# Kernel tuning notes

Measured on AMD Instinct MI355X. Metric: run time of the kernel, lower is better.

Reference implementation:

```python
import jax, jax.numpy as jnp
import numpy as np

B, C, IN_LEN, OUT_LEN, E, TOP_K, N_I = 1, 8192, 512, 512, 8, 2, 16


def setup_inputs() -> dict:
    key = jax.random.key(0)
    ks = jax.random.split(key, 8)
    w = lambda k, shape, sc=0.02: jax.random.normal(k, shape, dtype=jnp.float32) * sc
    return {
        "x": jax.random.normal(ks[0], (B, C, IN_LEN), dtype=jnp.float32),
        "Ins_tk": jax.random.normal(ks[1], (B, N_I, OUT_LEN), dtype=jnp.float32),
        "gate_w": w(ks[2], (IN_LEN, E)),            # Gate: Linear(in_len, E, bias=False)
        "expert_w": w(ks[3], (E, IN_LEN, OUT_LEN)),  # per-expert Linear weight (transposed)
        "expert_b": jnp.zeros((E, OUT_LEN), dtype=jnp.float32),
        "gamma_w": w(ks[4], (E, OUT_LEN)),          # EiLM gamma_generator: Linear(h,1,bias=False)
        "beta_w": w(ks[5], (E, OUT_LEN, OUT_LEN)),  # EiLM beta_generator (transposed)
        "rmod_w": w(ks[6], (OUT_LEN, E)),           # router_modulator: Linear(out_len, E, bias=False)
    }


def reference(x, Ins_tk, gate_w, expert_w, expert_b, gamma_w, beta_w, rmod_w):
    Bx, Cx, L = x.shape
    xf = x.reshape(-1, L)                                   # [N, in_len], N = B*C
    ins = Ins_tk[0]                                         # [N_i, out_len] (B==1 asserted)

    # Router: logits + expert-wise modulation of logits
    router_gamma = jnp.mean(ins @ rmod_w, axis=0)           # [E]
    logits = xf @ gate_w + router_gamma                     # [N, E]
    probs = jax.nn.softmax(logits.astype(jnp.float32), axis=-1)
    rw, sel = jax.lax.top_k(probs, TOP_K)                   # [N, k] values/indices (no renorm)

    # Combine weights per token per expert: sum_k rw[t,k] * onehot(sel[t,k])
    combine = jnp.sum(jax.nn.one_hot(sel, E, dtype=rw.dtype) * rw[..., None], axis=1)  # [N, E]

    # EiLM per-expert affine params: scalar gamma, vector beta (mean over instruction tokens)
    gam = jnp.mean(ins @ gamma_w.T, axis=0)                 # [E]
    bet = jnp.einsum('nh,ehd->ed', ins, beta_w) / N_I       # [E, out_len]

    # Per-expert linear over all tokens, then EiLM modulation
    eo = jnp.einsum('nl,eld->end', xf, expert_w) + expert_b[:, None, :]   # [E, N, out]
    mod = gam[:, None, None] * eo + bet[:, None, :]                        # [E, N, out]

    out = jnp.einsum('ne,end->nd', combine, mod)            # [N, out]
    return out.reshape(Bx, Cx, OUT_LEN)
```

## Files before the change

kernel.cpp:

```cpp
#include <hip/hip_runtime.h>
#include <hip/hip_bf16.h>

#define N_TOK 8192
#define INL   512
#define OUTL  512
#define NE    8
#define NI    16

typedef unsigned short ushort_t;
typedef unsigned int   uint_t;
typedef short  short8  __attribute__((ext_vector_type(8)));
typedef float  floatx4 __attribute__((ext_vector_type(4)));

#define WS_S      0u
#define WS_GAM    2048u
#define WS_RGAM   2080u
#define WS_BET    2112u
#define WS_SELE   18496u
#define WS_SELW   51264u
#define WS_WT     182336u

__device__ __forceinline__ ushort_t f2bf(float f) {
    uint_t b = __float_as_uint(f);
    return (ushort_t)((b + 0x7FFFu + ((b >> 16) & 1u)) >> 16);
}
__device__ __forceinline__ uint_t pkbf(float a, float b) {
    __hip_bfloat162 h = __float22bfloat162_rn(make_float2(a, b));
    union { __hip_bfloat162 h2; uint_t u; } cv;
    cv.h2 = h;
    return cv.u;
}
__device__ __forceinline__ void dma16(const ushort_t* g, ushort_t* l) {
    __builtin_amdgcn_global_load_lds(
        (const __attribute__((address_space(1))) void*)g,
        (__attribute__((address_space(3))) void*)l,
        16, 0, 0);
}

__global__ void k_stats(const float* __restrict__ ins,
                        const float* __restrict__ gamma_w,
                        const float* __restrict__ rmod_w,
                        float* __restrict__ wsS, float* __restrict__ wsGam,
                        float* __restrict__ wsRgam) {
    __shared__ float sS[INL];
    __shared__ float pg[64], pr[64];
    int tid = threadIdx.x;
    for (int h = tid; h < INL; h += 256) {
        float a = 0.f;
        for (int n = 0; n < NI; ++n) a += ins[n * INL + h];
        sS[h] = a;
        wsS[h] = a;
    }
    __syncthreads();
    if (tid < 64) {
        int e = tid & 7, qq = tid >> 3;
        float g = 0.f, r = 0.f;
        for (int j = 0; j < 64; ++j) {
            int h = qq * 64 + j;
            float sv = sS[h];
            g += sv * gamma_w[e * INL + h];
            r += sv * rmod_w[h * NE + e];
        }
        pg[tid] = g; pr[tid] = r;
    }
    __syncthreads();
    if (tid < NE) {
        float g = 0.f, r = 0.f;
        for (int qq = 0; qq < 8; ++qq) { g += pg[qq * 8 + tid]; r += pr[qq * 8 + tid]; }
        wsGam[tid]  = g * (1.f / NI);
        wsRgam[tid] = r * (1.f / NI);
    }
}

__global__ void k_bet(const float* __restrict__ ins,
                      const float* __restrict__ gamma_w,
                      const float* __restrict__ beta_w,
                      const float* __restrict__ expert_b,
                      float* __restrict__ wsBet) {
    __shared__ float sS[INL];
    __shared__ float red[256];
    __shared__ float gamS;
    int e = blockIdx.y;
    int dBase = blockIdx.x * 32;
    int tid = threadIdx.x;
    for (int h = tid; h < INL; h += 256) {
        float a = 0.f;
        for (int n = 0; n < NI; ++n) a += ins[n * INL + h];
        sS[h] = a;
    }
    __syncthreads();
    if (tid < 64) {
        float g = 0.f;
        for (int j = 0; j < 8; ++j) g += sS[tid * 8 + j] * gamma_w[e * INL + tid * 8 + j];
        for (int off = 32; off >= 1; off >>= 1) g += __shfl_xor(g, off, 64);
        if (tid == 0) gamS = g * (1.f / NI);
    }
    int doff = tid & 31, hq = tid >> 5;
    float a = 0.f;
    for (int j = 0; j < 64; ++j) {
        int h = hq * 64 + j;
        a += sS[h] * beta_w[(e * INL + h) * OUTL + dBase + doff];
    }
    red[tid] = a;
    __syncthreads();
    if (tid < 32) {
        float t = 0.f;
        for (int k = 0; k < 8; ++k) t += red[k * 32 + tid];
        int d = dBase + tid;
        wsBet[e * OUTL + d] = t * (1.f / NI) + gamS * expert_b[e * OUTL + d];
    }
}

__global__ void k_route(const float* __restrict__ x,
                        const float* __restrict__ gate_w,
                        const float* __restrict__ wsGam,
                        const float* __restrict__ wsRgam,
                        int* __restrict__ selE, float4* __restrict__ selW) {
    __shared__ float gateT[NE * INL];
    int tid = threadIdx.x;
    for (int i = 0; i < 16; ++i) {
        int f = tid + 256 * i;
        float v = gate_w[f];
        gateT[(f & 7) * INL + (f >> 3)] = v;
    }
    __syncthreads();

    int w = tid >> 6, lane = tid & 63;
    int tbase = blockIdx.x * 16 + w * 4;

    for (int tt = 0; tt < 4; ++tt) {
        int t = tbase + tt;
        float2 xv[4];
        for (int i = 0; i < 4; ++i)
            xv[i] = *(const float2*)(x + (size_t)t * INL + 2 * lane + 128 * i);

        float acc[NE];
        for (int e = 0; e < NE; ++e) acc[e] = 0.f;
        for (int i = 0; i < 4; ++i) {
            int c = 2 * lane + 128 * i;
            for (int e = 0; e < NE; ++e)
                acc[e] += xv[i].x * gateT[e * INL + c] + xv[i].y * gateT[e * INL + c + 1];
        }
        for (int e = 0; e < NE; ++e) {
            float a = acc[e];
            for (int off = 32; off >= 1; off >>= 1) a += __shfl_xor(a, off, 64);
            acc[e] = a;
        }
        float logit[NE];
        for (int e = 0; e < NE; ++e) logit[e] = acc[e] + wsRgam[e];

        int i0 = 0; float m0 = logit[0];
        for (int e = 1; e < NE; ++e) if (logit[e] > m0) { m0 = logit[e]; i0 = e; }
        int i1 = -1; float m1 = -3.4e38f;
        for (int e = 0; e < NE; ++e) if (e != i0 && logit[e] > m1) { m1 = logit[e]; i1 = e; }

        float S = 0.f;
        for (int e = 0; e < NE; ++e) S += expf(logit[e] - m0);
        float rw0 = 1.0f / S;
        float rw1 = expf(m1 - m0) / S;

        if (lane == 0) {
            selE[t] = i0 | (i1 << 8);
            selW[t] = make_float4(rw0 * wsGam[i0], rw1 * wsGam[i1], rw0, rw1);
        }
    }
}

__global__ void k_wt(const float* __restrict__ expert_w, ushort_t* __restrict__ wt) {
    __shared__ float tile[64][65];
    int e = blockIdx.z;
    int lt = blockIdx.y * 64, dt = blockIdx.x * 64;
    int tid = threadIdx.x;
    int dIdx = tid & 63, lq = tid >> 6;
    for (int i = 0; i < 16; ++i) {
        int l = lq * 16 + i;
        tile[l][dIdx] = expert_w[(e * INL + lt + l) * OUTL + dt + dIdx];
    }
    __syncthreads();
    int lIdx = tid & 63, dq = tid >> 6;
    for (int i = 0; i < 16; ++i) {
        int d = dq * 16 + i;
        wt[(e * OUTL + dt + d) * INL + lt + lIdx] = f2bf(tile[lIdx][d]);
    }
}

__global__ __launch_bounds__(256, 2)
void k_gemm(const float* __restrict__ x, const ushort_t* __restrict__ wt,
            const int* __restrict__ selE, const float4* __restrict__ selW,
            const float* __restrict__ wsBet, float* __restrict__ out) {
    int bx = blockIdx.x;
    int rt = bx & 63;
    int ct = bx >> 6;
    __shared__ ushort_t Blds[2][64 * 64];

    int tid = threadIdx.x;
    int wid = tid >> 6, lane = tid & 63;
    int wm = wid * 32;
    int mrow = lane & 15, laneq = lane >> 4, q8 = laneq * 8, qr = laneq * 4;

    float wv[2][NE];
    for (int mt = 0; mt < 2; ++mt) {
        int tok = rt * 128 + wm + mt * 16 + mrow;
        int es = selE[tok];
        float4 w4 = selW[tok];
        int e0 = es & 255, e1 = es >> 8;
        for (int e = 0; e < NE; ++e)
            wv[mt][e] = (e == e0) ? w4.x : ((e == e1) ? w4.y : 0.f);
    }

    const float* arow[2];
    for (int mt = 0; mt < 2; ++mt)
        arow[mt] = x + (size_t)(rt * 128 + wm + mt * 16 + mrow) * INL + q8;

    int c0 = tid, c1 = tid + 256;
    int col0 = c0 >> 3, kg0 = ((c0 & 7) - col0) & 7;
    int col1 = c1 >> 3, kg1 = ((c1 & 7) - col1) & 7;
    const ushort_t* pB0 = wt + (size_t)(ct * 64 + col0) * INL + kg0 * 8;
    const ushort_t* pB1 = wt + (size_t)(ct * 64 + col1) * INL + kg1 * 8;
    ushort_t* ldsW0;
    ushort_t* ldsW1;
    {
        int base0 = (wid * 64) * 8;
        int base1 = (256 + wid * 64) * 8;
        ldsW0 = &Blds[0][0] + base0;
        ldsW1 = &Blds[0][0] + base1;
    }

    int fcol[4], frot0[4];
    for (int nt = 0; nt < 4; ++nt) {
        fcol[nt] = nt * 16 + mrow;
        frot0[nt] = (laneq + fcol[nt]) & 7;
    }

    floatx4 comb[2][4];
    for (int mt = 0; mt < 2; ++mt)
        for (int nt = 0; nt < 4; ++nt)
            comb[mt][nt] = (floatx4){0.f, 0.f, 0.f, 0.f};

    dma16(pB0, ldsW0);
    dma16(pB1, ldsW1);
    __syncthreads();

    float4 ar[2][2][2];

    #pragma unroll 1
    for (int kc = 0; kc < 8; ++kc) {
        for (int mt = 0; mt < 2; ++mt)
            for (int ks = 0; ks < 2; ++ks) {
                const float* p = arow[mt] + kc * 64 + ks * 32;
                ar[mt][ks][0] = *(const float4*)p;
                ar[mt][ks][1] = *(const float4*)(p + 4);
            }

        #pragma unroll
        for (int e = 0; e < NE; ++e) {
            int step = kc * 8 + e;
            int buf = step & 1;
            int ne = e + 1, nkc = kc;
            if (ne == NE) { ne = 0; nkc = kc + 1; }
            if (nkc < 8) {
                size_t off = (size_t)ne * (OUTL * INL) + (size_t)nkc * 64;
                int nb = (step + 1) & 1;
                dma16(pB0 + off, ldsW0 + nb * (64 * 64));
                dma16(pB1 + off, ldsW1 + nb * (64 * 64));
            }

            const ushort_t* B = &Blds[buf][0];
            short8 bf[4][2];
            for (int nt = 0; nt < 4; ++nt) {
                int cb = fcol[nt] * 64;
                bf[nt][0] = *(const short8*)&B[cb + frot0[nt] * 8];
                bf[nt][1] = *(const short8*)&B[cb + ((frot0[nt] + 4) & 7) * 8];
            }
            for (int mt = 0; mt < 2; ++mt) {
                float w = wv[mt][e];
                for (int ks = 0; ks < 2; ++ks) {
                    union { uint4 u; short8 s; } af;
                    float4 a0 = ar[mt][ks][0], a1 = ar[mt][ks][1];
                    af.u.x = pkbf(a0.x * w, a0.y * w);
                    af.u.y = pkbf(a0.z * w, a0.w * w);
                    af.u.z = pkbf(a1.x * w, a1.y * w);
                    af.u.w = pkbf(a1.z * w, a1.w * w);
                    for (int nt = 0; nt < 4; ++nt)
                        comb[mt][nt] = __builtin_amdgcn_mfma_f32_16x16x32_bf16(
                            af.s, bf[nt][ks], comb[mt][nt], 0, 0, 0);
                }
            }
            __syncthreads();
        }
    }

    for (int mt = 0; mt < 2; ++mt) {
        for (int ri = 0; ri < 4; ++ri) {
            int row = wm + mt * 16 + qr + ri;
            int tok = rt * 128 + row;
            int es = selE[tok];
            float4 w4 = selW[tok];
            int e0 = es & 255, e1 = es >> 8;
            for (int nt = 0; nt < 4; ++nt) {
                int col = ct * 64 + nt * 16 + mrow;
                float bet = w4.z * wsBet[e0 * OUTL + col] + w4.w * wsBet[e1 * OUTL + col];
                out[(size_t)tok * OUTL + col] = comb[mt][nt][ri] + bet;
            }
        }
    }
}

extern "C" void kernel_launch(void* const* d_in, const int* in_sizes, int n_in,
                              void* d_out, int out_size, void* d_ws, size_t ws_size,
                              hipStream_t stream) {
    const float* x        = (const float*)d_in[0];
    const float* ins      = (const float*)d_in[1];
    const float* gate_w   = (const float*)d_in[2];
    const float* expert_w = (const float*)d_in[3];
    const float* expert_b = (const float*)d_in[4];
    const float* gamma_w  = (const float*)d_in[5];
    const float* beta_w   = (const float*)d_in[6];
    const float* rmod_w   = (const float*)d_in[7];
    float* out = (float*)d_out;

    char* ws = (char*)d_ws;
    float*    wsS    = (float*)(ws + WS_S);
    float*    wsGam  = (float*)(ws + WS_GAM);
    float*    wsRgam = (float*)(ws + WS_RGAM);
    float*    wsBet  = (float*)(ws + WS_BET);
    int*      selE   = (int*)(ws + WS_SELE);
    float4*   selW   = (float4*)(ws + WS_SELW);
    ushort_t* wt     = (ushort_t*)(ws + WS_WT);

    k_stats<<<1, 256, 0, stream>>>(ins, gamma_w, rmod_w, wsS, wsGam, wsRgam);
    k_wt<<<dim3(8, 8, 8), 256, 0, stream>>>(expert_w, wt);
    k_bet<<<dim3(16, 8), 256, 0, stream>>>(ins, gamma_w, beta_w, expert_b, wsBet);
    k_route<<<N_TOK / 16, 256, 0, stream>>>(x, gate_w, wsGam, wsRgam, selE, selW);
    k_gemm<<<512, 256, 0, stream>>>(x, wt, selE, selW, wsBet, out);
}
```

Baseline: 160.5 us.

## Merge prep kernels into one launch and widen GEMM pipeline to four experts per stage

The four preprocessing kernels (stats, beta, routing, weight transpose) are folded into a single launch that dispatches on block index, and each routing block now recomputes the router and gamma statistics locally. This removes three launches and the serial dependency between them. The GEMM now stages four experts' weight tiles per double-buffered step, giving 16 steps instead of 64. That means fewer barriers and an A-row prefetch one step ahead, at the cost of 64KB of LDS per block, which may lower occupancy. There is a redundant duplicate initial A-load.

```diff
diff --git a/kernel.cpp b/kernel.cpp
--- a/kernel.cpp
+++ b/kernel.cpp
@@ -6,15 +6,13 @@
 #define OUTL  512
 #define NE    8
 #define NI    16
+#define EOFF  (OUTL * INL)
 
 typedef unsigned short ushort_t;
 typedef unsigned int   uint_t;
 typedef short  short8  __attribute__((ext_vector_type(8)));
 typedef float  floatx4 __attribute__((ext_vector_type(4)));
 
-#define WS_S      0u
-#define WS_GAM    2048u
-#define WS_RGAM   2080u
 #define WS_BET    2112u
 #define WS_SELE   18496u
 #define WS_SELW   51264u
@@ -37,19 +35,92 @@
         16, 0, 0);
 }
 
-__global__ void k_stats(const float* __restrict__ ins,
-                        const float* __restrict__ gamma_w,
-                        const float* __restrict__ rmod_w,
-                        float* __restrict__ wsS, float* __restrict__ wsGam,
-                        float* __restrict__ wsRgam) {
-    __shared__ float sS[INL];
-    __shared__ float pg[64], pr[64];
+__global__ __launch_bounds__(256)
+void k_prep(const float* __restrict__ x,
+            const float* __restrict__ ins,
+            const float* __restrict__ gate_w,
+            const float* __restrict__ expert_w,
+            const float* __restrict__ expert_b,
+            const float* __restrict__ gamma_w,
+            const float* __restrict__ beta_w,
+            const float* __restrict__ rmod_w,
+            ushort_t* __restrict__ wt,
+            float* __restrict__ wsBet,
+            int* __restrict__ selE, float4* __restrict__ selW) {
+    __shared__ __align__(16) char smem[19072];
+    int bx = blockIdx.x;
     int tid = threadIdx.x;
+
+    if (bx < 512) {
+        float (*tile)[65] = (float(*)[65])smem;
+        int e = bx >> 6, rem = bx & 63;
+        int lt = (rem >> 3) * 64, dt = (rem & 7) * 64;
+        int dIdx = tid & 63, lq = tid >> 6;
+        for (int i = 0; i < 16; ++i) {
+            int l = lq * 16 + i;
+            tile[l][dIdx] = expert_w[(e * INL + lt + l) * OUTL + dt + dIdx];
+        }
+        __syncthreads();
+        int lIdx = tid & 63, dq = tid >> 6;
+        for (int i = 0; i < 16; ++i) {
+            int d = dq * 16 + i;
+            wt[(e * OUTL + dt + d) * INL + lt + lIdx] = f2bf(tile[lIdx][d]);
+        }
+        return;
+    }
+
+    if (bx < 640) {
+        float* sS  = (float*)smem;
+        float* red = sS + 512;
+        float* gamS = red + 256;
+        int b2 = bx - 512;
+        int e = b2 >> 4, dBase = (b2 & 15) * 32;
+        for (int h = tid; h < INL; h += 256) {
+            float a = 0.f;
+            for (int n = 0; n < NI; ++n) a += ins[n * INL + h];
+            sS[h] = a;
+        }
+        __syncthreads();
+        if (tid < 64) {
+            float g = 0.f;
+            for (int j = 0; j < 8; ++j) g += sS[tid * 8 + j] * gamma_w[e * INL + tid * 8 + j];
+            for (int off = 32; off >= 1; off >>= 1) g += __shfl_xor(g, off, 64);
+            if (tid == 0) gamS[0] = g * (1.f / NI);
+        }
+        int doff = tid & 31, hq = tid >> 5;
+        float a = 0.f;
+        for (int j = 0; j < 64; ++j) {
+            int h = hq * 64 + j;
+            a += sS[h] * beta_w[(e * INL + h) * OUTL + dBase + doff];
+        }
+        red[tid] = a;
+        __syncthreads();
+        if (tid < 32) {
+            float t = 0.f;
+            for (int k = 0; k < 8; ++k) t += red[k * 32 + tid];
+            int d = dBase + tid;
+            wsBet[e * OUTL + d] = t * (1.f / NI) + gamS[0] * expert_b[e * OUTL + d];
+        }
+        return;
+    }
+
+    float* gateT = (float*)smem;
+    float* sS    = gateT + NE * INL;
+    float* pg    = sS + 512;
+    float* pr    = pg + 64;
+    float* gg    = pr + 64;
+    float* rg    = gg + 8;
+    int rb = bx - 640;
+
+    for (int i = 0; i < 16; ++i) {
+        int f = tid + 256 * i;
+        float v = gate_w[f];
+        gateT[(f & 7) * INL + (f >> 3)] = v;
+    }
     for (int h = tid; h < INL; h += 256) {
         float a = 0.f;
         for (int n = 0; n < NI; ++n) a += ins[n * INL + h];
         sS[h] = a;
-        wsS[h] = a;
     }
     __syncthreads();
     if (tid < 64) {
@@ -67,67 +138,13 @@
     if (tid < NE) {
         float g = 0.f, r = 0.f;
         for (int qq = 0; qq < 8; ++qq) { g += pg[qq * 8 + tid]; r += pr[qq * 8 + tid]; }
-        wsGam[tid]  = g * (1.f / NI);
-        wsRgam[tid] = r * (1.f / NI);
-    }
-}
-
-__global__ void k_bet(const float* __restrict__ ins,
-                      const float* __restrict__ gamma_w,
-                      const float* __restrict__ beta_w,
-                      const float* __restrict__ expert_b,
-                      float* __restrict__ wsBet) {
-    __shared__ float sS[INL];
-    __shared__ float red[256];
-    __shared__ float gamS;
-    int e = blockIdx.y;
-    int dBase = blockIdx.x * 32;
-    int tid = threadIdx.x;
-    for (int h = tid; h < INL; h += 256) {
-        float a = 0.f;
-        for (int n = 0; n < NI; ++n) a += ins[n * INL + h];
-        sS[h] = a;
+        gg[tid] = g * (1.f / NI);
+        rg[tid] = r * (1.f / NI);
     }
     __syncthreads();
-    if (tid < 64) {
-        float g = 0.f;
-        for (int j = 0; j < 8; ++j) g += sS[tid * 8 + j] * gamma_w[e * INL + tid * 8 + j];
-        for (int off = 32; off >= 1; off >>= 1) g += __shfl_xor(g, off, 64);
-        if (tid == 0) gamS = g * (1.f / NI);
-    }
-    int doff = tid & 31, hq = tid >> 5;
-    float a = 0.f;
-    for (int j = 0; j < 64; ++j) {
-        int h = hq * 64 + j;
-        a += sS[h] * beta_w[(e * INL + h) * OUTL + dBase + doff];
-    }
-    red[tid] = a;
-    __syncthreads();
-    if (tid < 32) {
-        float t = 0.f;
-        for (int k = 0; k < 8; ++k) t += red[k * 32 + tid];
-        int d = dBase + tid;
-        wsBet[e * OUTL + d] = t * (1.f / NI) + gamS * expert_b[e * OUTL + d];
-    }
-}
-
-__global__ void k_route(const float* __restrict__ x,
-                        const float* __restrict__ gate_w,
-                        const float* __restrict__ wsGam,
-                        const float* __restrict__ wsRgam,
-                        int* __restrict__ selE, float4* __restrict__ selW) {
-    __shared__ float gateT[NE * INL];
-    int tid = threadIdx.x;
-    for (int i = 0; i < 16; ++i) {
-        int f = tid + 256 * i;
-        float v = gate_w[f];
-        gateT[(f & 7) * INL + (f >> 3)] = v;
-    }
-    __syncthreads();
 
     int w = tid >> 6, lane = tid & 63;
-    int tbase = blockIdx.x * 16 + w * 4;
-
+    int tbase = rb * 16 + w * 4;
     for (int tt = 0; tt < 4; ++tt) {
         int t = tbase + tt;
         float2 xv[4];
@@ -147,7 +164,7 @@
             acc[e] = a;
         }
         float logit[NE];
-        for (int e = 0; e < NE; ++e) logit[e] = acc[e] + wsRgam[e];
+        for (int e = 0; e < NE; ++e) logit[e] = acc[e] + rg[e];
 
         int i0 = 0; float m0 = logit[0];
         for (int e = 1; e < NE; ++e) if (logit[e] > m0) { m0 = logit[e]; i0 = e; }
@@ -161,26 +178,8 @@
 
         if (lane == 0) {
             selE[t] = i0 | (i1 << 8);
-            selW[t] = make_float4(rw0 * wsGam[i0], rw1 * wsGam[i1], rw0, rw1);
-        }
-    }
-}
-
-__global__ void k_wt(const float* __restrict__ expert_w, ushort_t* __restrict__ wt) {
-    __shared__ float tile[64][65];
-    int e = blockIdx.z;
-    int lt = blockIdx.y * 64, dt = blockIdx.x * 64;
-    int tid = threadIdx.x;
-    int dIdx = tid & 63, lq = tid >> 6;
-    for (int i = 0; i < 16; ++i) {
-        int l = lq * 16 + i;
-        tile[l][dIdx] = expert_w[(e * INL + lt + l) * OUTL + dt + dIdx];
-    }
-    __syncthreads();
-    int lIdx = tid & 63, dq = tid >> 6;
-    for (int i = 0; i < 16; ++i) {
-        int d = dq * 16 + i;
-        wt[(e * OUTL + dt + d) * INL + lt + lIdx] = f2bf(tile[lIdx][d]);
+            selW[t] = make_float4(rw0 * gg[i0], rw1 * gg[i1], rw0, rw1);
+        }
     }
 }
 
@@ -191,7 +190,7 @@
     int bx = blockIdx.x;
     int rt = bx & 63;
     int ct = bx >> 6;
-    __shared__ ushort_t Blds[2][64 * 64];
+    __shared__ ushort_t Blds[2 * 4 * 4096];
 
     int tid = threadIdx.x;
     int wid = tid >> 6, lane = tid & 63;
@@ -217,14 +216,8 @@
     int col1 = c1 >> 3, kg1 = ((c1 & 7) - col1) & 7;
     const ushort_t* pB0 = wt + (size_t)(ct * 64 + col0) * INL + kg0 * 8;
     const ushort_t* pB1 = wt + (size_t)(ct * 64 + col1) * INL + kg1 * 8;
-    ushort_t* ldsW0;
-    ushort_t* ldsW1;
-    {
-        int base0 = (wid * 64) * 8;
-        int base1 = (256 + wid * 64) * 8;
-        ldsW0 = &Blds[0][0] + base0;
-        ldsW1 = &Blds[0][0] + base1;
-    }
+    ushort_t* ldsW0 = &Blds[0] + (wid * 64) * 8;
+    ushort_t* ldsW1 = &Blds[0] + (256 + wid * 64) * 8;
 
     int fcol[4], frot0[4];
     for (int nt = 0; nt < 4; ++nt) {
@@ -237,35 +230,54 @@
         for (int nt = 0; nt < 4; ++nt)
             comb[mt][nt] = (floatx4){0.f, 0.f, 0.f, 0.f};
 
-    dma16(pB0, ldsW0);
-    dma16(pB1, ldsW1);
-    __syncthreads();
-
+    for (int ei = 0; ei < 4; ++ei) {
+        size_t off = (size_t)ei * EOFF;
+        dma16(pB0 + off, ldsW0 + ei * 4096);
+        dma16(pB1 + off, ldsW1 + ei * 4096);
+    }
     float4 ar[2][2][2];
+    for (int mt = 0; mt < 2; ++mt)
+        for (int ks = 0; ks < 2; ++ks) {
+            ar[mt][ks][0] = *(const float4*)(arow[mt]);
+            ar[mt][ks][1] = *(const float4*)(arow[mt] + 4);
+        }
+    for (int mt = 0; mt < 2; ++mt)
+        for (int ks = 0; ks < 2; ++ks) {
+            const float* p = arow[mt] + ks * 32;
+            ar[mt][ks][0] = *(const float4*)p;
+            ar[mt][ks][1] = *(const float4*)(p + 4);
+        }
 
     #pragma unroll 1
-    for (int kc = 0; kc < 8; ++kc) {
-        for (int mt = 0; mt < 2; ++mt)
-            for (int ks = 0; ks < 2; ++ks) {
-                const float* p = arow[mt] + kc * 64 + ks * 32;
-                ar[mt][ks][0] = *(const float4*)p;
-                ar[mt][ks][1] = *(const float4*)(p + 4);
+    for (int step = 0; step < 16; ++step) {
+        int buf = step & 1;
+        int kc = step >> 1, eh = step & 1;
+        __syncthreads();
+
+        if (step < 15) {
+            int ns = step + 1;
+            int nkc = ns >> 1, neh = ns & 1, nb = ns & 1;
+            for (int ei = 0; ei < 4; ++ei) {
+                size_t off = (size_t)(neh * 4 + ei) * EOFF + (size_t)nkc * 64;
+                dma16(pB0 + off, ldsW0 + nb * 16384 + ei * 4096);
+                dma16(pB1 + off, ldsW1 + nb * 16384 + ei * 4096);
             }
+        }
+        float4 arn[2][2][2];
+        bool haveArn = (eh == 1 && kc < 7);
+        if (haveArn) {
+            for (int mt = 0; mt < 2; ++mt)
+                for (int ks = 0; ks < 2; ++ks) {
+                    const float* p = arow[mt] + (kc + 1) * 64 + ks * 32;
+                    arn[mt][ks][0] = *(const float4*)p;
+                    arn[mt][ks][1] = *(const float4*)(p + 4);
+                }
+        }
 
         #pragma unroll
-        for (int e = 0; e < NE; ++e) {
-            int step = kc * 8 + e;
-            int buf = step & 1;
-            int ne = e + 1, nkc = kc;
-            if (ne == NE) { ne = 0; nkc = kc + 1; }
-            if (nkc < 8) {
-                size_t off = (size_t)ne * (OUTL * INL) + (size_t)nkc * 64;
-                int nb = (step + 1) & 1;
-                dma16(pB0 + off, ldsW0 + nb * (64 * 64));
-                dma16(pB1 + off, ldsW1 + nb * (64 * 64));
-            }
-
-            const ushort_t* B = &Blds[buf][0];
+        for (int ei = 0; ei < 4; ++ei) {
+            int e = eh * 4 + ei;
+            const ushort_t* B = &Blds[buf * 16384 + ei * 4096];
             short8 bf[4][2];
             for (int nt = 0; nt < 4; ++nt) {
                 int cb = fcol[nt] * 64;
@@ -286,7 +298,11 @@
                             af.s, bf[nt][ks], comb[mt][nt], 0, 0, 0);
                 }
             }
-            __syncthreads();
+        }
+        if (haveArn) {
+            for (int mt = 0; mt < 2; ++mt)
+                for (int ks = 0; ks < 2; ++ks)
+                    for (int h = 0; h < 2; ++h) ar[mt][ks][h] = arn[mt][ks][h];
         }
     }
 
@@ -320,17 +336,13 @@
     float* out = (float*)d_out;
 
     char* ws = (char*)d_ws;
-    float*    wsS    = (float*)(ws + WS_S);
-    float*    wsGam  = (float*)(ws + WS_GAM);
-    float*    wsRgam = (float*)(ws + WS_RGAM);
     float*    wsBet  = (float*)(ws + WS_BET);
     int*      selE   = (int*)(ws + WS_SELE);
     float4*   selW   = (float4*)(ws + WS_SELW);
     ushort_t* wt     = (ushort_t*)(ws + WS_WT);
 
-    k_stats<<<1, 256, 0, stream>>>(ins, gamma_w, rmod_w, wsS, wsGam, wsRgam);
-    k_wt<<<dim3(8, 8, 8), 256, 0, stream>>>(expert_w, wt);
-    k_bet<<<dim3(16, 8), 256, 0, stream>>>(ins, gamma_w, beta_w, expert_b, wsBet);
-    k_route<<<N_TOK / 16, 256, 0, stream>>>(x, gate_w, wsGam, wsRgam, selE, selW);
+    k_prep<<<1152, 256, 0, stream>>>(x, ins, gate_w, expert_w, expert_b,
+                                     gamma_w, beta_w, rmod_w,
+                                     wt, wsBet, selE, selW);
     k_gemm<<<512, 256, 0, stream>>>(x, wt, selE, selW, wsBet, out);
 }
```

Result: slower. 172.0 us (+7.2%).

## Merge prep kernels into one launch and halve GEMM row tile

Applied to the files above, without the earlier changes.

The three setup kernels (stats, bias/beta generation, expert-weight transpose to bf16) are folded into a single k_prep launch whose block index picks the role. This saves two launches and lets the independent work run concurrently. The GEMM row tile shrinks from 128 to 64 tokens (one 16-row MFMA tile per wave), which doubles the grid to 1024 blocks and raises the occupancy hint to 4. In exchange, each B tile loaded into LDS is reused by half as many rows, so weight traffic doubles.

```diff
diff --git a/kernel.cpp b/kernel.cpp
--- a/kernel.cpp
+++ b/kernel.cpp
@@ -6,13 +6,13 @@
 #define OUTL  512
 #define NE    8
 #define NI    16
+#define EOFF  (OUTL * INL)
 
 typedef unsigned short ushort_t;
 typedef unsigned int   uint_t;
 typedef short  short8  __attribute__((ext_vector_type(8)));
 typedef float  floatx4 __attribute__((ext_vector_type(4)));
 
-#define WS_S      0u
 #define WS_GAM    2048u
 #define WS_RGAM   2080u
 #define WS_BET    2112u
@@ -37,77 +37,101 @@
         16, 0, 0);
 }
 
-__global__ void k_stats(const float* __restrict__ ins,
-                        const float* __restrict__ gamma_w,
-                        const float* __restrict__ rmod_w,
-                        float* __restrict__ wsS, float* __restrict__ wsGam,
-                        float* __restrict__ wsRgam) {
-    __shared__ float sS[INL];
-    __shared__ float pg[64], pr[64];
+__global__ __launch_bounds__(256)
+void k_prep(const float* __restrict__ ins,
+            const float* __restrict__ expert_w,
+            const float* __restrict__ expert_b,
+            const float* __restrict__ gamma_w,
+            const float* __restrict__ beta_w,
+            const float* __restrict__ rmod_w,
+            ushort_t* __restrict__ wt,
+            float* __restrict__ wsBet,
+            float* __restrict__ wsGam, float* __restrict__ wsRgam) {
+    __shared__ __align__(16) char smem[17152];
+    int bx = blockIdx.x;
     int tid = threadIdx.x;
-    for (int h = tid; h < INL; h += 256) {
+
+    if (bx < 512) {
+        float (*tile)[65] = (float(*)[65])smem;
+        int e = bx >> 6, rem = bx & 63;
+        int lt = (rem >> 3) * 64, dt = (rem & 7) * 64;
+        int dIdx = tid & 63, lq = tid >> 6;
+        for (int i = 0; i < 16; ++i) {
+            int l = lq * 16 + i;
+            tile[l][dIdx] = expert_w[(e * INL + lt + l) * OUTL + dt + dIdx];
+        }
+        __syncthreads();
+        int lIdx = tid & 63, dq = tid >> 6;
+        for (int i = 0; i < 16; ++i) {
+            int d = dq * 16 + i;
+            wt[(e * OUTL + dt + d) * INL + lt + lIdx] = f2bf(tile[lIdx][d]);
+        }
+        return;
+    }
+
+    if (bx < 640) {
+        float* sS  = (float*)smem;
+        float* red = sS + 512;
+        float* gamS = red + 256;
+        int b2 = bx - 512;
+        int e = b2 >> 4, dBase = (b2 & 15) * 32;
+        for (int h = tid; h < INL; h += 256) {
+            float a = 0.f;
+            for (int n = 0; n < NI; ++n) a += ins[n * INL + h];
+            sS[h] = a;
+        }
+        __syncthreads();
+        if (tid < 64) {
+            float g = 0.f;
+            for (int j = 0; j < 8; ++j) g += sS[tid * 8 + j] * gamma_w[e * INL + tid * 8 + j];
+            for (int off = 32; off >= 1; off >>= 1) g += __shfl_xor(g, off, 64);
+            if (tid == 0) gamS[0] = g * (1.f / NI);
+        }
+        int doff = tid & 31, hq = tid >> 5;
         float a = 0.f;
-        for (int n = 0; n < NI; ++n) a += ins[n * INL + h];
-        sS[h] = a;
-        wsS[h] = a;
-    }
-    __syncthreads();
-    if (tid < 64) {
-        int e = tid & 7, qq = tid >> 3;
-        float g = 0.f, r = 0.f;
         for (int j = 0; j < 64; ++j) {
-            int h = qq * 64 + j;
-            float sv = sS[h];
-            g += sv * gamma_w[e * INL + h];
-            r += sv * rmod_w[h * NE + e];
-        }
-        pg[tid] = g; pr[tid] = r;
-    }
-    __syncthreads();
-    if (tid < NE) {
-        float g = 0.f, r = 0.f;
-        for (int qq = 0; qq < 8; ++qq) { g += pg[qq * 8 + tid]; r += pr[qq * 8 + tid]; }
-        wsGam[tid]  = g * (1.f / NI);
-        wsRgam[tid] = r * (1.f / NI);
-    }
-}
-
-__global__ void k_bet(const float* __restrict__ ins,
-                      const float* __restrict__ gamma_w,
-                      const float* __restrict__ beta_w,
-                      const float* __restrict__ expert_b,
-                      float* __restrict__ wsBet) {
-    __shared__ float sS[INL];
-    __shared__ float red[256];
-    __shared__ float gamS;
-    int e = blockIdx.y;
-    int dBase = blockIdx.x * 32;
-    int tid = threadIdx.x;
-    for (int h = tid; h < INL; h += 256) {
-        float a = 0.f;
-        for (int n = 0; n < NI; ++n) a += ins[n * INL + h];
-        sS[h] = a;
-    }
-    __syncthreads();
-    if (tid < 64) {
-        float g = 0.f;
-        for (int j = 0; j < 8; ++j) g += sS[tid * 8 + j] * gamma_w[e * INL + tid * 8 + j];
-        for (int off = 32; off >= 1; off >>= 1) g += __shfl_xor(g, off, 64);
-        if (tid == 0) gamS = g * (1.f / NI);
-    }
-    int doff = tid & 31, hq = tid >> 5;
-    float a = 0.f;
-    for (int j = 0; j < 64; ++j) {
-        int h = hq * 64 + j;
-        a += sS[h] * beta_w[(e * INL + h) * OUTL + dBase + doff];
-    }
-    red[tid] = a;
-    __syncthreads();
-    if (tid < 32) {
-        float t = 0.f;
-        for (int k = 0; k < 8; ++k) t += red[k * 32 + tid];
-        int d = dBase + tid;
-        wsBet[e * OUTL + d] = t * (1.f / NI) + gamS * expert_b[e * OUTL + d];
+            int h = hq * 64 + j;
+            a += sS[h] * beta_w[(e * INL + h) * OUTL + dBase + doff];
+        }
+        red[tid] = a;
+        __syncthreads();
+        if (tid < 32) {
+            float t = 0.f;
+            for (int k = 0; k < 8; ++k) t += red[k * 32 + tid];
+            int d = dBase + tid;
+            wsBet[e * OUTL + d] = t * (1.f / NI) + gamS[0] * expert_b[e * OUTL + d];
+        }
+        return;
+    }
+
+    {
+        float* sS = (float*)smem;
+        float* pg = sS + 512;
+        float* pr = pg + 64;
+        for (int h = tid; h < INL; h += 256) {
+            float a = 0.f;
+            for (int n = 0; n < NI; ++n) a += ins[n * INL + h];
+            sS[h] = a;
+        }
+        __syncthreads();
+        if (tid < 64) {
+            int e = tid & 7, qq = tid >> 3;
+            float g = 0.f, r = 0.f;
+            for (int j = 0; j < 64; ++j) {
+                int h = qq * 64 + j;
+                float sv = sS[h];
+                g += sv * gamma_w[e * INL + h];
+                r += sv * rmod_w[h * NE + e];
+            }
+            pg[tid] = g; pr[tid] = r;
+        }
+        __syncthreads();
+        if (tid < NE) {
+            float g = 0.f, r = 0.f;
+            for (int qq = 0; qq < 8; ++qq) { g += pg[qq * 8 + tid]; r += pr[qq * 8 + tid]; }
+            wsGam[tid]  = g * (1.f / NI);
+            wsRgam[tid] = r * (1.f / NI);
+        }
     }
 }
 
@@ -166,65 +190,38 @@
     }
 }
 
-__global__ void k_wt(const float* __restrict__ expert_w, ushort_t* __restrict__ wt) {
-    __shared__ float tile[64][65];
-    int e = blockIdx.z;
-    int lt = blockIdx.y * 64, dt = blockIdx.x * 64;
-    int tid = threadIdx.x;
-    int dIdx = tid & 63, lq = tid >> 6;
-    for (int i = 0; i < 16; ++i) {
-        int l = lq * 16 + i;
-        tile[l][dIdx] = expert_w[(e * INL + lt + l) * OUTL + dt + dIdx];
-    }
-    __syncthreads();
-    int lIdx = tid & 63, dq = tid >> 6;
-    for (int i = 0; i < 16; ++i) {
-        int d = dq * 16 + i;
-        wt[(e * OUTL + dt + d) * INL + lt + lIdx] = f2bf(tile[lIdx][d]);
-    }
-}
-
-__global__ __launch_bounds__(256, 2)
+__global__ __launch_bounds__(256, 4)
 void k_gemm(const float* __restrict__ x, const ushort_t* __restrict__ wt,
             const int* __restrict__ selE, const float4* __restrict__ selW,
             const float* __restrict__ wsBet, float* __restrict__ out) {
     int bx = blockIdx.x;
-    int rt = bx & 63;
-    int ct = bx >> 6;
+    int rt = bx & 127;
+    int ct = bx >> 7;
     __shared__ ushort_t Blds[2][64 * 64];
 
     int tid = threadIdx.x;
     int wid = tid >> 6, lane = tid & 63;
-    int wm = wid * 32;
+    int wm = wid * 16;
     int mrow = lane & 15, laneq = lane >> 4, q8 = laneq * 8, qr = laneq * 4;
 
-    float wv[2][NE];
-    for (int mt = 0; mt < 2; ++mt) {
-        int tok = rt * 128 + wm + mt * 16 + mrow;
-        int es = selE[tok];
-        float4 w4 = selW[tok];
+    int tokL = rt * 64 + wm + mrow;
+    float wv[NE];
+    {
+        int es = selE[tokL];
+        float4 w4 = selW[tokL];
         int e0 = es & 255, e1 = es >> 8;
         for (int e = 0; e < NE; ++e)
-            wv[mt][e] = (e == e0) ? w4.x : ((e == e1) ? w4.y : 0.f);
-    }
-
-    const float* arow[2];
-    for (int mt = 0; mt < 2; ++mt)
-        arow[mt] = x + (size_t)(rt * 128 + wm + mt * 16 + mrow) * INL + q8;
+            wv[e] = (e == e0) ? w4.x : ((e == e1) ? w4.y : 0.f);
+    }
+    const float* arowp = x + (size_t)tokL * INL + q8;
 
     int c0 = tid, c1 = tid + 256;
     int col0 = c0 >> 3, kg0 = ((c0 & 7) - col0) & 7;
     int col1 = c1 >> 3, kg1 = ((c1 & 7) - col1) & 7;
     const ushort_t* pB0 = wt + (size_t)(ct * 64 + col0) * INL + kg0 * 8;
     const ushort_t* pB1 = wt + (size_t)(ct * 64 + col1) * INL + kg1 * 8;
-    ushort_t* ldsW0;
-    ushort_t* ldsW1;
-    {
-        int base0 = (wid * 64) * 8;
-        int base1 = (256 + wid * 64) * 8;
-        ldsW0 = &Blds[0][0] + base0;
-        ldsW1 = &Blds[0][0] + base1;
-    }
+    ushort_t* ldsW0 = &Blds[0][0] + (wid * 64) * 8;
+    ushort_t* ldsW1 = &Blds[0][0] + (256 + wid * 64) * 8;
 
     int fcol[4], frot0[4];
     for (int nt = 0; nt < 4; ++nt) {
@@ -232,25 +229,22 @@
         frot0[nt] = (laneq + fcol[nt]) & 7;
     }
 
-    floatx4 comb[2][4];
-    for (int mt = 0; mt < 2; ++mt)
-        for (int nt = 0; nt < 4; ++nt)
-            comb[mt][nt] = (floatx4){0.f, 0.f, 0.f, 0.f};
+    floatx4 comb[4];
+    for (int nt = 0; nt < 4; ++nt) comb[nt] = (floatx4){0.f, 0.f, 0.f, 0.f};
 
     dma16(pB0, ldsW0);
     dma16(pB1, ldsW1);
     __syncthreads();
 
-    float4 ar[2][2][2];
+    float4 ar[2][2];
 
     #pragma unroll 1
     for (int kc = 0; kc < 8; ++kc) {
-        for (int mt = 0; mt < 2; ++mt)
-            for (int ks = 0; ks < 2; ++ks) {
-                const float* p = arow[mt] + kc * 64 + ks * 32;
-                ar[mt][ks][0] = *(const float4*)p;
-                ar[mt][ks][1] = *(const float4*)(p + 4);
-            }
+        for (int ks = 0; ks < 2; ++ks) {
+            const float* p = arowp + kc * 64 + ks * 32;
+            ar[ks][0] = *(const float4*)p;
+            ar[ks][1] = *(const float4*)(p + 4);
+        }
 
         #pragma unroll
         for (int e = 0; e < NE; ++e) {
@@ -259,10 +253,10 @@
             int ne = e + 1, nkc = kc;
             if (ne == NE) { ne = 0; nkc = kc + 1; }
             if (nkc < 8) {
-                size_t off = (size_t)ne * (OUTL * INL) + (size_t)nkc * 64;
+                size_t off = (size_t)ne * EOFF + (size_t)nkc * 64;
                 int nb = (step + 1) & 1;
-                dma16(pB0 + off, ldsW0 + nb * (64 * 64));
-                dma16(pB1 + off, ldsW1 + nb * (64 * 64));
+                dma16(pB0 + off, ldsW0 + nb * 4096);
+                dma16(pB1 + off, ldsW1 + nb * 4096);
             }
 
             const ushort_t* B = &Blds[buf][0];
@@ -272,36 +266,32 @@
                 bf[nt][0] = *(const short8*)&B[cb + frot0[nt] * 8];
                 bf[nt][1] = *(const short8*)&B[cb + ((frot0[nt] + 4) & 7) * 8];
             }
-            for (int mt = 0; mt < 2; ++mt) {
-                float w = wv[mt][e];
-                for (int ks = 0; ks < 2; ++ks) {
-                    union { uint4 u; short8 s; } af;
-                    float4 a0 = ar[mt][ks][0], a1 = ar[mt][ks][1];
-                    af.u.x = pkbf(a0.x * w, a0.y * w);
-                    af.u.y = pkbf(a0.z * w, a0.w * w);
-                    af.u.z = pkbf(a1.x * w, a1.y * w);
-                    af.u.w = pkbf(a1.z * w, a1.w * w);
-                    for (int nt = 0; nt < 4; ++nt)
-                        comb[mt][nt] = __builtin_amdgcn_mfma_f32_16x16x32_bf16(
-                            af.s, bf[nt][ks], comb[mt][nt], 0, 0, 0);
-                }
+            float w = wv[e];
+            for (int ks = 0; ks < 2; ++ks) {
+                union { uint4 u; short8 s; } af;
+                float4 a0 = ar[ks][0], a1 = ar[ks][1];
+                af.u.x = pkbf(a0.x * w, a0.y * w);
+                af.u.y = pkbf(a0.z * w, a0.w * w);
+                af.u.z = pkbf(a1.x * w, a1.y * w);
+                af.u.w = pkbf(a1.z * w, a1.w * w);
+                for (int nt = 0; nt < 4; ++nt)
+                    comb[nt] = __builtin_amdgcn_mfma_f32_16x16x32_bf16(
+                        af.s, bf[nt][ks], comb[nt], 0, 0, 0);
             }
             __syncthreads();
         }
     }
 
-    for (int mt = 0; mt < 2; ++mt) {
-        for (int ri = 0; ri < 4; ++ri) {
-            int row = wm + mt * 16 + qr + ri;
-            int tok = rt * 128 + row;
-            int es = selE[tok];
-            float4 w4 = selW[tok];
-            int e0 = es & 255, e1 = es >> 8;
-            for (int nt = 0; nt < 4; ++nt) {
-                int col = ct * 64 + nt * 16 + mrow;
-                float bet = w4.z * wsBet[e0 * OUTL + col] + w4.w * wsBet[e1 * OUTL + col];
-                out[(size_t)tok * OUTL + col] = comb[mt][nt][ri] + bet;
-            }
+    for (int ri = 0; ri < 4; ++ri) {
+        int row = wm + qr + ri;
+        int tok = rt * 64 + row;
+        int es = selE[tok];
+        float4 w4 = selW[tok];
+        int e0 = es & 255, e1 = es >> 8;
+        for (int nt = 0; nt < 4; ++nt) {
+            int col = ct * 64 + nt * 16 + mrow;
+            float bet = w4.z * wsBet[e0 * OUTL + col] + w4.w * wsBet[e1 * OUTL + col];
+            out[(size_t)tok * OUTL + col] = comb[nt][ri] + bet;
         }
     }
 }
@@ -320,7 +310,6 @@
     float* out = (float*)d_out;
 
     char* ws = (char*)d_ws;
-    float*    wsS    = (float*)(ws + WS_S);
     float*    wsGam  = (float*)(ws + WS_GAM);
     float*    wsRgam = (float*)(ws + WS_RGAM);
     float*    wsBet  = (float*)(ws + WS_BET);
@@ -328,9 +317,9 @@
     float4*   selW   = (float4*)(ws + WS_SELW);
     ushort_t* wt     = (ushort_t*)(ws + WS_WT);
 
-    k_stats<<<1, 256, 0, stream>>>(ins, gamma_w, rmod_w, wsS, wsGam, wsRgam);
-    k_wt<<<dim3(8, 8, 8), 256, 0, stream>>>(expert_w, wt);
-    k_bet<<<dim3(16, 8), 256, 0, stream>>>(ins, gamma_w, beta_w, expert_b, wsBet);
+    k_prep<<<641, 256, 0, stream>>>(ins, expert_w, expert_b,
+                                    gamma_w, beta_w, rmod_w,
+                                    wt, wsBet, wsGam, wsRgam);
     k_route<<<N_TOK / 16, 256, 0, stream>>>(x, gate_w, wsGam, wsRgam, selE, selW);
-    k_gemm<<<512, 256, 0, stream>>>(x, wt, selE, selW, wsBet, out);
-}
+    k_gemm<<<1024, 256, 0, stream>>>(x, wt, selE, selW, wsBet, out);
+}
```

New measurement: 150.8 us. -6.0%, faster.
